# Optimization experiments

Hardware: AMD Instinct MI355X
Metric: run time of the kernel (lower is better)

The kernel has to match this reference:

```python
import jax, jax.numpy as jnp
import numpy as np

V, E = 50000, 300        # vocab, word2vec embedding dim
B, T = 64, 512           # batch, sequence length
U1, U2, DD = 64, 32, 32  # brnn1 units, brnn2 units, dense units


def _glorot(k, shape):
    lim = np.sqrt(6.0 / (shape[0] + shape[1])).astype(np.float32)
    return jax.random.uniform(k, shape, jnp.float32, -lim, lim)


def setup_inputs() -> dict:
    key = jax.random.key(0)
    ks = jax.random.split(key, 12)
    return {
        "token_ids": jax.random.randint(ks[0], (B, T), 0, V),
        "emb": jax.random.normal(ks[1], (V, E), jnp.float32) * 0.05,
        # per-cell gate weights stacked [f|i|c|o] along output dim (same math as 4 separate matmuls)
        "w1f": _glorot(ks[2], (E + U1, 4 * U1)), "b1f": jnp.zeros((4 * U1,), jnp.float32),
        "w1b": _glorot(ks[3], (E + U1, 4 * U1)), "b1b": jnp.zeros((4 * U1,), jnp.float32),
        "w2f": _glorot(ks[4], (2 * U1 + U2, 4 * U2)), "b2f": jnp.zeros((4 * U2,), jnp.float32),
        "w2b": _glorot(ks[5], (2 * U1 + U2, 4 * U2)), "b2b": jnp.zeros((4 * U2,), jnp.float32),
        "wd": _glorot(ks[6], (2 * U2, DD)), "bd": jnp.zeros((DD,), jnp.float32),
        "wo": _glorot(ks[7], (DD, 1)), "bo": jnp.zeros((1,), jnp.float32),
    }


def _lstm(xs, W, b, units, reverse=False):
    # xs: (T, B, D). Single fused gate matmul per step; scan carries (h, c).
    h0 = jnp.zeros((xs.shape[1], units), xs.dtype)
    c0 = jnp.zeros_like(h0)

    def step(carry, x_t):
        h, c = carry
        z = jnp.concatenate([x_t, h], axis=-1) @ W + b  # (B, 4U)
        f, i, g, o = jnp.split(z, 4, axis=-1)
        f = jax.nn.sigmoid(f)
        i = jax.nn.sigmoid(i)
        g = jnp.tanh(g)
        o = jax.nn.sigmoid(o)
        c_new = f * c + i * g
        h_new = o * jnp.tanh(c_new)
        return (h_new, c_new), h_new

    (hT, _), ys = jax.lax.scan(step, (h0, c0), xs, reverse=reverse)
    return ys, hT  # ys: (T, B, U) in original time order; hT = final hidden


def reference(token_ids, emb, w1f, b1f, w1b, b1b, w2f, b2f, w2b, b2b, wd, bd, wo, bo):
    x = emb[token_ids]                      # (B, T, E) frozen word2vec lookup
    xs = jnp.transpose(x, (1, 0, 2))        # (T, B, E)
    # BRNN layer 1: return_sequences=True, merge='concat'
    yf, _ = _lstm(xs, w1f, b1f, U1)
    yb, _ = _lstm(xs, w1b, b1b, U1, reverse=True)
    h1 = jnp.concatenate([yf, yb], axis=-1)  # (T, B, 2*U1); dropout1 = identity at inference
    # BRNN layer 2: return_sequences=False -> final fwd h and final bwd h, concat
    _, hf = _lstm(h1, w2f, b2f, U2)
    _, hb = _lstm(h1, w2b, b2b, U2, reverse=True)
    h2 = jnp.concatenate([hf, hb], axis=-1)  # (B, 2*U2)
    d = jax.nn.relu(h2 @ wd + bd)            # dense head; dropout2 = identity
    return jax.nn.sigmoid(d @ wo + bo)       # (B, 1) sentiment probability
```

## Files before the change

kernel.cpp:

```cpp
#include <hip/hip_runtime.h>

#define T_LEN 512
#define B_SZ  64

typedef _Float16 h2_t  __attribute__((ext_vector_type(2)));
typedef _Float16 f16x8 __attribute__((ext_vector_type(8)));
typedef float    f32x4 __attribute__((ext_vector_type(4)));

#if defined(__has_builtin)
#  if __has_builtin(__builtin_amdgcn_fdot2)
#    define FDOT2(a, b, c) __builtin_amdgcn_fdot2((a), (b), (c), false)
#  endif
#endif
#ifndef FDOT2
__device__ __forceinline__ float fdot2_fb(h2_t a, h2_t b, float c) {
    return fmaf((float)a[0], (float)b[0], fmaf((float)a[1], (float)b[1], c));
}
#  define FDOT2(a, b, c) fdot2_fb((a), (b), (c))
#endif

__device__ __forceinline__ float sigf(float x) {
    return 1.0f / (1.0f + __expf(-x));
}
__device__ __forceinline__ float tanhf_(float x) {
    return 2.0f / (1.0f + __expf(-2.0f * x)) - 1.0f;
}
__device__ __forceinline__ unsigned pack2(float x, float y) {
    h2_t p; p[0] = (_Float16)x; p[1] = (_Float16)y;
    return __builtin_bit_cast(unsigned, p);
}

__device__ __forceinline__ void lds_barrier() {
    asm volatile("s_waitcnt lgkmcnt(0)" ::: "memory");
    __builtin_amdgcn_s_barrier();
    asm volatile("" ::: "memory");
}

__global__ __launch_bounds__(64) void prep_w1(
    const float* __restrict__ w1f, const float* __restrict__ w1b,
    _Float16* __restrict__ Wt1)
{
    const int col = blockIdx.x;
    const int t   = threadIdx.x;
    if (t >= 40) return;
    const float* __restrict__ W = (col < 256) ? w1f : w1b;
    const int c = col & 255;
    f16x8 v;
    #pragma unroll
    for (int i = 0; i < 8; ++i) {
        int k = t * 8 + i;
        float x = (k < 300) ? W[(size_t)k * 256 + c] : 0.0f;
        v[i] = (_Float16)x;
    }
    *(f16x8*)(Wt1 + (size_t)col * 320 + t * 8) = v;
}

__global__ __launch_bounds__(64) void prep_w2(
    const float* __restrict__ w2f, const float* __restrict__ w2b,
    _Float16* __restrict__ Wt2)
{
    const int col = blockIdx.x;
    const int t   = threadIdx.x;
    if (t >= 16) return;
    const float* __restrict__ W = (col < 128) ? w2f : w2b;
    const int c = col & 127;
    f16x8 v;
    #pragma unroll
    for (int i = 0; i < 8; ++i) {
        int k = t * 8 + i;
        v[i] = (_Float16)W[(size_t)k * 128 + c];
    }
    *(f16x8*)(Wt2 + (size_t)col * 128 + t * 8) = v;
}

__global__ __launch_bounds__(256, 1) void gemm1_kernel(
    const int* __restrict__ tok, const float* __restrict__ emb,
    const _Float16* __restrict__ Wt1,
    const float* __restrict__ b1f, const float* __restrict__ b1b,
    float* __restrict__ Z1)
{
    const int row0 = blockIdx.x * 64;
    const int b    = row0 >> 9;
    const int t0   = row0 & 511;
    const int tid  = threadIdx.x;

    __shared__ __align__(16) _Float16 A_lds[64][328];

    {
        const int row = tid >> 2, q = tid & 3;
        const int tk = tok[b * T_LEN + t0 + row];
        const float* __restrict__ src = emb + (size_t)tk * 300 + q * 80;
        #pragma unroll
        for (int i = 0; i < 20; ++i) {
            float4 v;
            if (q == 3 && i >= 15) v = make_float4(0.f, 0.f, 0.f, 0.f);
            else                   v = *(const float4*)(src + i * 4);
            uint2 u; u.x = pack2(v.x, v.y); u.y = pack2(v.z, v.w);
            *(uint2*)&A_lds[row][q * 80 + i * 4] = u;
        }
    }
    __syncthreads();

    const int l   = tid & 63;
    const int w   = tid >> 6;
    const int wN0 = w * 128;
    const int lr  = l & 15;
    const int lk8 = (l >> 4) * 8;

    f32x4 acc[4][8] = {};

    #pragma unroll 2
    for (int ks = 0; ks < 10; ++ks) {
        const int k0 = ks * 32;
        f16x8 af[4];
        #pragma unroll
        for (int m = 0; m < 4; ++m)
            af[m] = *(const f16x8*)&A_lds[m * 16 + lr][k0 + lk8];
        f16x8 bf[8];
        #pragma unroll
        for (int n = 0; n < 8; ++n)
            bf[n] = *(const f16x8*)(Wt1 + (size_t)(wN0 + n * 16 + lr) * 320 + k0 + lk8);
        #pragma unroll
        for (int m = 0; m < 4; ++m)
            #pragma unroll
            for (int n = 0; n < 8; ++n)
                acc[m][n] = __builtin_amdgcn_mfma_f32_16x16x32_f16(af[m], bf[n], acc[m][n], 0, 0, 0);
    }

    const int dir = wN0 >> 8;
    const int rq  = (l >> 4) * 4;
    #pragma unroll
    for (int n = 0; n < 8; ++n) {
        const int colr = (wN0 + n * 16 + lr) & 255;
        const float bv = dir ? b1b[colr] : b1f[colr];
        #pragma unroll
        for (int m = 0; m < 4; ++m) {
            const size_t rb = (size_t)dir * 32768 + row0 + m * 16 + rq;
            #pragma unroll
            for (int r = 0; r < 4; ++r)
                Z1[(rb + r) * 256 + colr] = acc[m][n][r] + bv;
        }
    }
}

__global__ __launch_bounds__(256, 1) void gemm2_kernel(
    const float* __restrict__ H1,
    const _Float16* __restrict__ Wt2,
    const float* __restrict__ b2f, const float* __restrict__ b2b,
    float* __restrict__ Z2)
{
    const int row0 = blockIdx.x * 64;
    const int tid  = threadIdx.x;

    __shared__ __align__(16) _Float16 A_lds[64][136];

    {
        const int row = tid >> 2, q = tid & 3;
        const float* __restrict__ src = H1 + (size_t)(row0 + row) * 128 + q * 32;
        #pragma unroll
        for (int i = 0; i < 8; ++i) {
            float4 v = *(const float4*)(src + i * 4);
            uint2 u; u.x = pack2(v.x, v.y); u.y = pack2(v.z, v.w);
            *(uint2*)&A_lds[row][q * 32 + i * 4] = u;
        }
    }
    __syncthreads();

    const int l   = tid & 63;
    const int w   = tid >> 6;
    const int wN0 = w * 64;
    const int lr  = l & 15;
    const int lk8 = (l >> 4) * 8;

    f32x4 acc[4][4] = {};

    #pragma unroll
    for (int ks = 0; ks < 4; ++ks) {
        const int k0 = ks * 32;
        f16x8 af[4];
        #pragma unroll
        for (int m = 0; m < 4; ++m)
            af[m] = *(const f16x8*)&A_lds[m * 16 + lr][k0 + lk8];
        f16x8 bf[4];
        #pragma unroll
        for (int n = 0; n < 4; ++n)
            bf[n] = *(const f16x8*)(Wt2 + (size_t)(wN0 + n * 16 + lr) * 128 + k0 + lk8);
        #pragma unroll
        for (int m = 0; m < 4; ++m)
            #pragma unroll
            for (int n = 0; n < 4; ++n)
                acc[m][n] = __builtin_amdgcn_mfma_f32_16x16x32_f16(af[m], bf[n], acc[m][n], 0, 0, 0);
    }

    const int dir = wN0 >> 7;
    const int rq  = (l >> 4) * 4;
    #pragma unroll
    for (int n = 0; n < 4; ++n) {
        const int colr = (wN0 + n * 16 + lr) & 127;
        const float bv = dir ? b2b[colr] : b2f[colr];
        #pragma unroll
        for (int m = 0; m < 4; ++m) {
            const size_t rb = (size_t)dir * 32768 + row0 + m * 16 + rq;
            #pragma unroll
            for (int r = 0; r < 4; ++r)
                Z2[(rb + r) * 128 + colr] = acc[m][n][r] + bv;
        }
    }
}

__global__ __launch_bounds__(256, 1) void lstm1_kernel(
    const float* __restrict__ Z1,
    const float* __restrict__ w1f, const float* __restrict__ w1b,
    float* __restrict__ H1)
{
    const int b   = blockIdx.x & 63;
    const int dir = blockIdx.x >> 6;
    const int tid = threadIdx.x;
    const int w   = tid >> 6;
    const int l   = tid & 63;
    const int ul  = l & 15;
    const int g   = (l >> 4) & 3;
    const int u   = w * 16 + ul;
    const int col = g * 64 + u;
    const float* __restrict__ W = dir ? w1b : w1f;

    h2_t wc[32];
    #pragma unroll
    for (int r = 0; r < 32; ++r) {
        float wa = W[(300 + 2 * r) * 256 + col];
        float wb = W[(301 + 2 * r) * 256 + col];
        h2_t p; p[0] = (_Float16)wa; p[1] = (_Float16)wb;
        wc[r] = p;
    }

    __shared__ __align__(16) _Float16 hbuf[2][64];
    if (g == 0) hbuf[0][u] = (_Float16)0.0f;
    lds_barrier();

    float c = 0.0f;

    const float* __restrict__ zcol =
        Z1 + ((size_t)(dir * 64 + b) * T_LEN) * 256 + col;

    float zr[4];
    #pragma unroll
    for (int q = 0; q < 4; ++q) {
        int t = dir ? (T_LEN - 1 - q) : q;
        zr[q] = zcol[(size_t)t * 256];
    }

    float* __restrict__ hout = H1 + (size_t)b * T_LEN * 128 + dir * 64 + u;

    const bool s0b = (g & 1) != 0, s1b = (g >> 1) != 0;
    const float km  = (g == 2) ? -2.0f : -1.0f;
    const float num = (g == 2) ?  2.0f :  1.0f;
    const float off = (g == 2) ?  1.0f :  0.0f;

    for (int sb = 0; sb < T_LEN; sb += 4) {
        #pragma unroll
        for (int q = 0; q < 4; ++q) {
            const int s = sb + q;
            const uint4* hb = (const uint4*)hbuf[s & 1];
            float a0 = zr[q], a1 = 0.f, a2 = 0.f, a3 = 0.f;
            #pragma unroll
            for (int k = 0; k < 8; ++k) {
                uint4 hq = hb[k];
                h2_t p0 = __builtin_bit_cast(h2_t, hq.x);
                h2_t p1 = __builtin_bit_cast(h2_t, hq.y);
                h2_t p2 = __builtin_bit_cast(h2_t, hq.z);
                h2_t p3 = __builtin_bit_cast(h2_t, hq.w);
                a0 = FDOT2(p0, wc[4 * k + 0], a0);
                a1 = FDOT2(p1, wc[4 * k + 1], a1);
                a2 = FDOT2(p2, wc[4 * k + 2], a2);
                a3 = FDOT2(p3, wc[4 * k + 3], a3);
            }
            float zz = (a0 + a1) + (a2 + a3);

            {
                int sp = s + 4; if (sp > T_LEN - 1) sp = T_LEN - 1;
                int tp = dir ? (T_LEN - 1 - sp) : sp;
                zr[q] = zcol[(size_t)tp * 256];
            }

            float e = __expf(km * zz);
            float A = num / (1.0f + e) - off;
            float B = __shfl_xor(A, 16);
            float C = __shfl_xor(A, 32);
            float D = __shfl_xor(B, 32);
            float f_ = s1b ? (s0b ? D : C) : (s0b ? B : A);
            float i_ = s1b ? (s0b ? C : D) : (s0b ? A : B);
            float g_ = s1b ? (s0b ? B : A) : (s0b ? D : C);
            float o_ = s1b ? (s0b ? A : B) : (s0b ? C : D);
            c = fmaf(f_, c, i_ * g_);
            float h = o_ * tanhf_(c);
            if (g == 0) {
                int t = dir ? (T_LEN - 1 - s) : s;
                hout[(size_t)t * 128] = h;
                hbuf[(s + 1) & 1][u] = (_Float16)h;
            }
            lds_barrier();
        }
    }
}

__global__ __launch_bounds__(128, 1) void lstm2_kernel(
    const float* __restrict__ Z2,
    const float* __restrict__ w2f, const float* __restrict__ w2b,
    float* __restrict__ H2)
{
    const int b   = blockIdx.x & 63;
    const int dir = blockIdx.x >> 6;
    const int tid = threadIdx.x;
    const int w   = tid >> 6;
    const int l   = tid & 63;
    const int ul  = l & 15;
    const int g   = (l >> 4) & 3;
    const int u   = w * 16 + ul;
    const int col = g * 32 + u;
    const float* __restrict__ W = dir ? w2b : w2f;

    h2_t wc[16];
    #pragma unroll
    for (int r = 0; r < 16; ++r) {
        float wa = W[(128 + 2 * r) * 128 + col];
        float wb = W[(129 + 2 * r) * 128 + col];
        h2_t p; p[0] = (_Float16)wa; p[1] = (_Float16)wb;
        wc[r] = p;
    }

    __shared__ __align__(16) _Float16 hbuf[2][32];
    if (g == 0) hbuf[0][u] = (_Float16)0.0f;
    lds_barrier();

    float c = 0.0f, h = 0.0f;

    const float* __restrict__ zcol =
        Z2 + ((size_t)(dir * 64 + b) * T_LEN) * 128 + col;

    float zr[4];
    #pragma unroll
    for (int q = 0; q < 4; ++q) {
        int t = dir ? (T_LEN - 1 - q) : q;
        zr[q] = zcol[(size_t)t * 128];
    }

    const bool s0b = (g & 1) != 0, s1b = (g >> 1) != 0;
    const float km  = (g == 2) ? -2.0f : -1.0f;
    const float num = (g == 2) ?  2.0f :  1.0f;
    const float off = (g == 2) ?  1.0f :  0.0f;

    for (int sb = 0; sb < T_LEN; sb += 4) {
        #pragma unroll
        for (int q = 0; q < 4; ++q) {
            const int s = sb + q;
            const uint4* hb = (const uint4*)hbuf[s & 1];
            float a0 = zr[q], a1 = 0.f, a2 = 0.f, a3 = 0.f;
            #pragma unroll
            for (int k = 0; k < 4; ++k) {
                uint4 hq = hb[k];
                h2_t p0 = __builtin_bit_cast(h2_t, hq.x);
                h2_t p1 = __builtin_bit_cast(h2_t, hq.y);
                h2_t p2 = __builtin_bit_cast(h2_t, hq.z);
                h2_t p3 = __builtin_bit_cast(h2_t, hq.w);
                a0 = FDOT2(p0, wc[4 * k + 0], a0);
                a1 = FDOT2(p1, wc[4 * k + 1], a1);
                a2 = FDOT2(p2, wc[4 * k + 2], a2);
                a3 = FDOT2(p3, wc[4 * k + 3], a3);
            }
            float zz = (a0 + a1) + (a2 + a3);

            {
                int sp = s + 4; if (sp > T_LEN - 1) sp = T_LEN - 1;
                int tp = dir ? (T_LEN - 1 - sp) : sp;
                zr[q] = zcol[(size_t)tp * 128];
            }

            float e = __expf(km * zz);
            float A = num / (1.0f + e) - off;
            float B = __shfl_xor(A, 16);
            float C = __shfl_xor(A, 32);
            float D = __shfl_xor(B, 32);
            float f_ = s1b ? (s0b ? D : C) : (s0b ? B : A);
            float i_ = s1b ? (s0b ? C : D) : (s0b ? A : B);
            float g_ = s1b ? (s0b ? B : A) : (s0b ? D : C);
            float o_ = s1b ? (s0b ? A : B) : (s0b ? C : D);
            c = fmaf(f_, c, i_ * g_);
            h = o_ * tanhf_(c);
            if (g == 0)
                hbuf[(s + 1) & 1][u] = (_Float16)h;
            lds_barrier();
        }
    }
    if (g == 0)
        H2[b * 64 + dir * 32 + u] = h;
}

__global__ __launch_bounds__(256) void head_kernel(
    const float* __restrict__ H2,
    const float* __restrict__ wd, const float* __restrict__ bd,
    const float* __restrict__ wo, const float* __restrict__ bo,
    float* __restrict__ out)
{
    const int tid = threadIdx.x;
    const int b = tid >> 2, qd = tid & 3;

    float hv[64];
    #pragma unroll
    for (int v = 0; v < 64; ++v) hv[v] = H2[b * 64 + v];

    float part = 0.0f;
    #pragma unroll
    for (int iq = 0; iq < 8; ++iq) {
        int i = qd * 8 + iq;
        float a = bd[i];
        #pragma unroll
        for (int v = 0; v < 64; ++v)
            a = fmaf(hv[v], wd[v * 32 + i], a);
        a = fmaxf(a, 0.0f);
        part = fmaf(a, wo[i], part);
    }

    __shared__ float ps[256];
    ps[tid] = part;
    __syncthreads();
    if (qd == 0) {
        float s = ps[tid] + ps[tid + 1] + ps[tid + 2] + ps[tid + 3];
        out[b] = sigf(s + bo[0]);
    }
}

extern "C" void kernel_launch(void* const* d_in, const int* in_sizes, int n_in,
                              void* d_out, int out_size, void* d_ws, size_t ws_size,
                              hipStream_t stream)
{
    const int*   tok = (const int*)  d_in[0];
    const float* emb = (const float*)d_in[1];
    const float* w1f = (const float*)d_in[2];
    const float* b1f = (const float*)d_in[3];
    const float* w1b = (const float*)d_in[4];
    const float* b1b = (const float*)d_in[5];
    const float* w2f = (const float*)d_in[6];
    const float* b2f = (const float*)d_in[7];
    const float* w2b = (const float*)d_in[8];
    const float* b2b = (const float*)d_in[9];
    const float* wd  = (const float*)d_in[10];
    const float* bd  = (const float*)d_in[11];
    const float* wo  = (const float*)d_in[12];
    const float* bo  = (const float*)d_in[13];
    float* out = (float*)d_out;

    float* Z1 = (float*)d_ws;
    float* H1 = Z1 + (size_t)2 * 64 * 512 * 256;
    float* H2 = H1 + (size_t)64 * 512 * 128;
    _Float16* Wt1 = (_Float16*)(H2 + 4096);
    _Float16* Wt2 = Wt1 + (size_t)512 * 320;
    float* Z2 = Z1;

    prep_w1<<<512, 64, 0, stream>>>(w1f, w1b, Wt1);
    prep_w2<<<256, 64, 0, stream>>>(w2f, w2b, Wt2);
    gemm1_kernel<<<512, 256, 0, stream>>>(tok, emb, Wt1, b1f, b1b, Z1);
    lstm1_kernel<<<128, 256, 0, stream>>>(Z1, w1f, w1b, H1);
    gemm2_kernel<<<512, 256, 0, stream>>>(H1, Wt2, b2f, b2b, Z2);
    lstm2_kernel<<<128, 128, 0, stream>>>(Z2, w2f, w2b, H2);
    head_kernel<<<1, 256, 0, stream>>>(H2, wd, bd, wo, bo, out);
}
```

Baseline: 424.7 us.

## Batch LSTM recurrences over 16 sequences with MFMA and gate-interleaved Z layout

```diff
diff --git a/kernel.cpp b/kernel.cpp
--- a/kernel.cpp
+++ b/kernel.cpp
@@ -1,24 +1,11 @@
 #include <hip/hip_runtime.h>
 
 #define T_LEN 512
-#define B_SZ  64
 
 typedef _Float16 h2_t  __attribute__((ext_vector_type(2)));
 typedef _Float16 f16x8 __attribute__((ext_vector_type(8)));
 typedef float    f32x4 __attribute__((ext_vector_type(4)));
 
-#if defined(__has_builtin)
-#  if __has_builtin(__builtin_amdgcn_fdot2)
-#    define FDOT2(a, b, c) __builtin_amdgcn_fdot2((a), (b), (c), false)
-#  endif
-#endif
-#ifndef FDOT2
-__device__ __forceinline__ float fdot2_fb(h2_t a, h2_t b, float c) {
-    return fmaf((float)a[0], (float)b[0], fmaf((float)a[1], (float)b[1], c));
-}
-#  define FDOT2(a, b, c) fdot2_fb((a), (b), (c))
-#endif
-
 __device__ __forceinline__ float sigf(float x) {
     return 1.0f / (1.0f + __expf(-x));
 }
@@ -28,6 +15,9 @@
 __device__ __forceinline__ unsigned pack2(float x, float y) {
     h2_t p; p[0] = (_Float16)x; p[1] = (_Float16)y;
     return __builtin_bit_cast(unsigned, p);
+}
+__device__ __forceinline__ f32x4 c4(float4 v) {
+    f32x4 r; r[0] = v.x; r[1] = v.y; r[2] = v.z; r[3] = v.w; return r;
 }
 
 __device__ __forceinline__ void lds_barrier() {
@@ -73,11 +63,36 @@
     *(f16x8*)(Wt2 + (size_t)col * 128 + t * 8) = v;
 }
 
+__global__ __launch_bounds__(64) void prep_whr1(
+    const float* __restrict__ w1f, const float* __restrict__ w1b,
+    _Float16* __restrict__ Whr1)
+{
+    const int x    = blockIdx.x;
+    const int dir  = x >> 8, colp = x & 255;
+    const int u = colp >> 2, g = colp & 3;
+    const int k = threadIdx.x;
+    const float* __restrict__ W = dir ? w1b : w1f;
+    Whr1[(size_t)x * 64 + k] = (_Float16)W[(size_t)(300 + k) * 256 + g * 64 + u];
+}
+
+__global__ __launch_bounds__(64) void prep_whr2(
+    const float* __restrict__ w2f, const float* __restrict__ w2b,
+    _Float16* __restrict__ Whr2)
+{
+    const int x    = blockIdx.x;
+    const int dir  = x >> 7, colp = x & 127;
+    const int u = colp >> 2, g = colp & 3;
+    const int k = threadIdx.x;
+    if (k >= 32) return;
+    const float* __restrict__ W = dir ? w2b : w2f;
+    Whr2[(size_t)x * 32 + k] = (_Float16)W[(size_t)(128 + k) * 128 + g * 32 + u];
+}
+
 __global__ __launch_bounds__(256, 1) void gemm1_kernel(
     const int* __restrict__ tok, const float* __restrict__ emb,
     const _Float16* __restrict__ Wt1,
     const float* __restrict__ b1f, const float* __restrict__ b1b,
-    float* __restrict__ Z1)
+    float* __restrict__ Z1p)
 {
     const int row0 = blockIdx.x * 64;
     const int b    = row0 >> 9;
@@ -128,41 +143,43 @@
     }
 
     const int dir = wN0 >> 8;
+    const int bg  = b >> 4, b16 = b & 15;
     const int rq  = (l >> 4) * 4;
+    float* __restrict__ zslab =
+        Z1p + (((size_t)(dir * 4 + bg) * 512 + t0) * 16 + b16) * 256;
     #pragma unroll
     for (int n = 0; n < 8; ++n) {
         const int colr = (wN0 + n * 16 + lr) & 255;
+        const int uu = colr & 63, gg = colr >> 6;
+        const int colp = uu * 4 + gg;
         const float bv = dir ? b1b[colr] : b1f[colr];
         #pragma unroll
-        for (int m = 0; m < 4; ++m) {
-            const size_t rb = (size_t)dir * 32768 + row0 + m * 16 + rq;
+        for (int m = 0; m < 4; ++m)
             #pragma unroll
             for (int r = 0; r < 4; ++r)
-                Z1[(rb + r) * 256 + colr] = acc[m][n][r] + bv;
-        }
+                zslab[(size_t)(m * 16 + rq + r) * 4096 + colp] = acc[m][n][r] + bv;
     }
 }
 
 __global__ __launch_bounds__(256, 1) void gemm2_kernel(
-    const float* __restrict__ H1,
+    const _Float16* __restrict__ H1f,
     const _Float16* __restrict__ Wt2,
     const float* __restrict__ b2f, const float* __restrict__ b2b,
-    float* __restrict__ Z2)
+    float* __restrict__ Z2p)
 {
     const int row0 = blockIdx.x * 64;
+    const int b    = row0 >> 9;
+    const int t0   = row0 & 511;
     const int tid  = threadIdx.x;
 
     __shared__ __align__(16) _Float16 A_lds[64][136];
 
     {
         const int row = tid >> 2, q = tid & 3;
-        const float* __restrict__ src = H1 + (size_t)(row0 + row) * 128 + q * 32;
-        #pragma unroll
-        for (int i = 0; i < 8; ++i) {
-            float4 v = *(const float4*)(src + i * 4);
-            uint2 u; u.x = pack2(v.x, v.y); u.y = pack2(v.z, v.w);
-            *(uint2*)&A_lds[row][q * 32 + i * 4] = u;
-        }
+        const _Float16* __restrict__ src = H1f + (size_t)(row0 + row) * 128 + q * 32;
+        #pragma unroll
+        for (int i = 0; i < 4; ++i)
+            *(f16x8*)&A_lds[row][q * 32 + i * 8] = *(const f16x8*)(src + i * 8);
     }
     __syncthreads();
 
@@ -193,206 +210,148 @@
     }
 
     const int dir = wN0 >> 7;
+    const int bg  = b >> 4, b16 = b & 15;
     const int rq  = (l >> 4) * 4;
+    float* __restrict__ zslab =
+        Z2p + (((size_t)(dir * 4 + bg) * 512 + t0) * 16 + b16) * 128;
     #pragma unroll
     for (int n = 0; n < 4; ++n) {
         const int colr = (wN0 + n * 16 + lr) & 127;
+        const int uu = colr & 31, gg = colr >> 5;
+        const int colp = uu * 4 + gg;
         const float bv = dir ? b2b[colr] : b2f[colr];
         #pragma unroll
-        for (int m = 0; m < 4; ++m) {
-            const size_t rb = (size_t)dir * 32768 + row0 + m * 16 + rq;
+        for (int m = 0; m < 4; ++m)
             #pragma unroll
             for (int r = 0; r < 4; ++r)
-                Z2[(rb + r) * 128 + colr] = acc[m][n][r] + bv;
-        }
-    }
-}
-
-__global__ __launch_bounds__(256, 1) void lstm1_kernel(
-    const float* __restrict__ Z1,
-    const float* __restrict__ w1f, const float* __restrict__ w1b,
-    float* __restrict__ H1)
-{
-    const int b   = blockIdx.x & 63;
-    const int dir = blockIdx.x >> 6;
+                zslab[(size_t)(m * 16 + rq + r) * 2048 + colp] = acc[m][n][r] + bv;
+    }
+}
+
+__global__ __launch_bounds__(512, 1) void lstm1_kernel(
+    const float* __restrict__ Z1p,
+    const _Float16* __restrict__ Whr1,
+    _Float16* __restrict__ H1f)
+{
+    const int bg  = blockIdx.x & 3;
+    const int dir = blockIdx.x >> 2;
     const int tid = threadIdx.x;
     const int w   = tid >> 6;
     const int l   = tid & 63;
-    const int ul  = l & 15;
-    const int g   = (l >> 4) & 3;
-    const int u   = w * 16 + ul;
-    const int col = g * 64 + u;
-    const float* __restrict__ W = dir ? w1b : w1f;
-
-    h2_t wc[32];
-    #pragma unroll
-    for (int r = 0; r < 32; ++r) {
-        float wa = W[(300 + 2 * r) * 256 + col];
-        float wb = W[(301 + 2 * r) * 256 + col];
-        h2_t p; p[0] = (_Float16)wa; p[1] = (_Float16)wb;
-        wc[r] = p;
-    }
-
-    __shared__ __align__(16) _Float16 hbuf[2][64];
-    if (g == 0) hbuf[0][u] = (_Float16)0.0f;
+    const int bb  = l & 15;
+    const int q   = l >> 4;
+
+    f16x8 af[2][2];
+    #pragma unroll
+    for (int tt = 0; tt < 2; ++tt) {
+        const int colp = (2 * w + tt) * 16 + bb;
+        #pragma unroll
+        for (int ks = 0; ks < 2; ++ks)
+            af[tt][ks] = *(const f16x8*)&Whr1[(size_t)(dir * 256 + colp) * 64 + ks * 32 + q * 8];
+    }
+
+    __shared__ __align__(16) _Float16 hbuf[2][16][72];
+    for (int i = tid; i < 2 * 16 * 72; i += 512) ((_Float16*)hbuf)[i] = (_Float16)0.0f;
     lds_barrier();
 
-    float c = 0.0f;
-
-    const float* __restrict__ zcol =
-        Z1 + ((size_t)(dir * 64 + b) * T_LEN) * 256 + col;
-
-    float zr[4];
-    #pragma unroll
-    for (int q = 0; q < 4; ++q) {
-        int t = dir ? (T_LEN - 1 - q) : q;
-        zr[q] = zcol[(size_t)t * 256];
-    }
-
-    float* __restrict__ hout = H1 + (size_t)b * T_LEN * 128 + dir * 64 + u;
-
-    const bool s0b = (g & 1) != 0, s1b = (g >> 1) != 0;
-    const float km  = (g == 2) ? -2.0f : -1.0f;
-    const float num = (g == 2) ?  2.0f :  1.0f;
-    const float off = (g == 2) ?  1.0f :  0.0f;
-
-    for (int sb = 0; sb < T_LEN; sb += 4) {
-        #pragma unroll
-        for (int q = 0; q < 4; ++q) {
-            const int s = sb + q;
-            const uint4* hb = (const uint4*)hbuf[s & 1];
-            float a0 = zr[q], a1 = 0.f, a2 = 0.f, a3 = 0.f;
-            #pragma unroll
-            for (int k = 0; k < 8; ++k) {
-                uint4 hq = hb[k];
-                h2_t p0 = __builtin_bit_cast(h2_t, hq.x);
-                h2_t p1 = __builtin_bit_cast(h2_t, hq.y);
-                h2_t p2 = __builtin_bit_cast(h2_t, hq.z);
-                h2_t p3 = __builtin_bit_cast(h2_t, hq.w);
-                a0 = FDOT2(p0, wc[4 * k + 0], a0);
-                a1 = FDOT2(p1, wc[4 * k + 1], a1);
-                a2 = FDOT2(p2, wc[4 * k + 2], a2);
-                a3 = FDOT2(p3, wc[4 * k + 3], a3);
-            }
-            float zz = (a0 + a1) + (a2 + a3);
-
-            {
-                int sp = s + 4; if (sp > T_LEN - 1) sp = T_LEN - 1;
-                int tp = dir ? (T_LEN - 1 - sp) : sp;
-                zr[q] = zcol[(size_t)tp * 256];
-            }
-
-            float e = __expf(km * zz);
-            float A = num / (1.0f + e) - off;
-            float B = __shfl_xor(A, 16);
-            float C = __shfl_xor(A, 32);
-            float D = __shfl_xor(B, 32);
-            float f_ = s1b ? (s0b ? D : C) : (s0b ? B : A);
-            float i_ = s1b ? (s0b ? C : D) : (s0b ? A : B);
-            float g_ = s1b ? (s0b ? B : A) : (s0b ? D : C);
-            float o_ = s1b ? (s0b ? A : B) : (s0b ? C : D);
-            c = fmaf(f_, c, i_ * g_);
-            float h = o_ * tanhf_(c);
-            if (g == 0) {
-                int t = dir ? (T_LEN - 1 - s) : s;
-                hout[(size_t)t * 128] = h;
-                hbuf[(s + 1) & 1][u] = (_Float16)h;
-            }
-            lds_barrier();
+    float cc0 = 0.0f, cc1 = 0.0f;
+
+    const size_t dslab = (size_t)(dir * 4 + bg) * 512;
+    const float* __restrict__ zb0 = Z1p + (dslab * 16 + bb) * 256 + (2 * w) * 16 + q * 4;
+    const float* __restrict__ zb1 = zb0 + 16;
+
+    float4 zr0[4], zr1[4];
+    #pragma unroll
+    for (int p = 0; p < 4; ++p) {
+        int t = dir ? (T_LEN - 1 - p) : p;
+        zr0[p] = *(const float4*)(zb0 + (size_t)t * 4096);
+        zr1[p] = *(const float4*)(zb1 + (size_t)t * 4096);
+    }
+
+    const int u0 = 8 * w + q, u1 = u0 + 4;
+    _Float16* __restrict__ hO = H1f + ((size_t)(bg * 16 + bb) * T_LEN) * 128 + dir * 64;
+
+    for (int s = 0; s < T_LEN; ++s) {
+        const int par = s & 1;
+        const int t = dir ? (T_LEN - 1 - s) : s;
+        f16x8 B0 = *(const f16x8*)&hbuf[par][bb][q * 8];
+        f16x8 B1 = *(const f16x8*)&hbuf[par][bb][32 + q * 8];
+        const int slot = s & 3;
+        f32x4 acc0 = __builtin_amdgcn_mfma_f32_16x16x32_f16(af[0][0], B0, c4(zr0[slot]), 0, 0, 0);
+        acc0 = __builtin_amdgcn_mfma_f32_16x16x32_f16(af[0][1], B1, acc0, 0, 0, 0);
+        f32x4 acc1 = __builtin_amdgcn_mfma_f32_16x16x32_f16(af[1][0], B0, c4(zr1[slot]), 0, 0, 0);
+        acc1 = __builtin_amdgcn_mfma_f32_16x16x32_f16(af[1][1], B1, acc1, 0, 0, 0);
+        {
+            int sp = s + 4; if (sp > T_LEN - 1) sp = T_LEN - 1;
+            int tp = dir ? (T_LEN - 1 - sp) : sp;
+            zr0[slot] = *(const float4*)(zb0 + (size_t)tp * 4096);
+            zr1[slot] = *(const float4*)(zb1 + (size_t)tp * 4096);
         }
-    }
-}
-
-__global__ __launch_bounds__(128, 1) void lstm2_kernel(
-    const float* __restrict__ Z2,
-    const float* __restrict__ w2f, const float* __restrict__ w2b,
+        float f0 = sigf(acc0[0]), i0 = sigf(acc0[1]), g0 = tanhf_(acc0[2]), o0 = sigf(acc0[3]);
+        cc0 = fmaf(f0, cc0, i0 * g0);
+        float h0 = o0 * tanhf_(cc0);
+        float f1 = sigf(acc1[0]), i1 = sigf(acc1[1]), g1 = tanhf_(acc1[2]), o1 = sigf(acc1[3]);
+        cc1 = fmaf(f1, cc1, i1 * g1);
+        float h1 = o1 * tanhf_(cc1);
+        hO[(size_t)t * 128 + u0] = (_Float16)h0;
+        hO[(size_t)t * 128 + u1] = (_Float16)h1;
+        hbuf[par ^ 1][bb][u0] = (_Float16)h0;
+        hbuf[par ^ 1][bb][u1] = (_Float16)h1;
+        lds_barrier();
+    }
+}
+
+__global__ __launch_bounds__(512, 1) void lstm2_kernel(
+    const float* __restrict__ Z2p,
+    const _Float16* __restrict__ Whr2,
     float* __restrict__ H2)
 {
-    const int b   = blockIdx.x & 63;
-    const int dir = blockIdx.x >> 6;
+    const int bg  = blockIdx.x & 3;
+    const int dir = blockIdx.x >> 2;
     const int tid = threadIdx.x;
     const int w   = tid >> 6;
     const int l   = tid & 63;
-    const int ul  = l & 15;
-    const int g   = (l >> 4) & 3;
-    const int u   = w * 16 + ul;
-    const int col = g * 32 + u;
-    const float* __restrict__ W = dir ? w2b : w2f;
-
-    h2_t wc[16];
-    #pragma unroll
-    for (int r = 0; r < 16; ++r) {
-        float wa = W[(128 + 2 * r) * 128 + col];
-        float wb = W[(129 + 2 * r) * 128 + col];
-        h2_t p; p[0] = (_Float16)wa; p[1] = (_Float16)wb;
-        wc[r] = p;
-    }
-
-    __shared__ __align__(16) _Float16 hbuf[2][32];
-    if (g == 0) hbuf[0][u] = (_Float16)0.0f;
+    const int bb  = l & 15;
+    const int q   = l >> 4;
+
+    const int colp = w * 16 + bb;
+    f16x8 af = *(const f16x8*)&Whr2[(size_t)(dir * 128 + colp) * 32 + q * 8];
+
+    __shared__ __align__(16) _Float16 hbuf[2][16][40];
+    for (int i = tid; i < 2 * 16 * 40; i += 512) ((_Float16*)hbuf)[i] = (_Float16)0.0f;
     lds_barrier();
 
-    float c = 0.0f, h = 0.0f;
-
-    const float* __restrict__ zcol =
-        Z2 + ((size_t)(dir * 64 + b) * T_LEN) * 128 + col;
-
-    float zr[4];
-    #pragma unroll
-    for (int q = 0; q < 4; ++q) {
-        int t = dir ? (T_LEN - 1 - q) : q;
-        zr[q] = zcol[(size_t)t * 128];
-    }
-
-    const bool s0b = (g & 1) != 0, s1b = (g >> 1) != 0;
-    const float km  = (g == 2) ? -2.0f : -1.0f;
-    const float num = (g == 2) ?  2.0f :  1.0f;
-    const float off = (g == 2) ?  1.0f :  0.0f;
-
-    for (int sb = 0; sb < T_LEN; sb += 4) {
-        #pragma unroll
-        for (int q = 0; q < 4; ++q) {
-            const int s = sb + q;
-            const uint4* hb = (const uint4*)hbuf[s & 1];
-            float a0 = zr[q], a1 = 0.f, a2 = 0.f, a3 = 0.f;
-            #pragma unroll
-            for (int k = 0; k < 4; ++k) {
-                uint4 hq = hb[k];
-                h2_t p0 = __builtin_bit_cast(h2_t, hq.x);
-                h2_t p1 = __builtin_bit_cast(h2_t, hq.y);
-                h2_t p2 = __builtin_bit_cast(h2_t, hq.z);
-                h2_t p3 = __builtin_bit_cast(h2_t, hq.w);
-                a0 = FDOT2(p0, wc[4 * k + 0], a0);
-                a1 = FDOT2(p1, wc[4 * k + 1], a1);
-                a2 = FDOT2(p2, wc[4 * k + 2], a2);
-                a3 = FDOT2(p3, wc[4 * k + 3], a3);
-            }
-            float zz = (a0 + a1) + (a2 + a3);
-
-            {
-                int sp = s + 4; if (sp > T_LEN - 1) sp = T_LEN - 1;
-                int tp = dir ? (T_LEN - 1 - sp) : sp;
-                zr[q] = zcol[(size_t)tp * 128];
-            }
-
-            float e = __expf(km * zz);
-            float A = num / (1.0f + e) - off;
-            float B = __shfl_xor(A, 16);
-            float C = __shfl_xor(A, 32);
-            float D = __shfl_xor(B, 32);
-            float f_ = s1b ? (s0b ? D : C) : (s0b ? B : A);
-            float i_ = s1b ? (s0b ? C : D) : (s0b ? A : B);
-            float g_ = s1b ? (s0b ? B : A) : (s0b ? D : C);
-            float o_ = s1b ? (s0b ? A : B) : (s0b ? C : D);
-            c = fmaf(f_, c, i_ * g_);
-            h = o_ * tanhf_(c);
-            if (g == 0)
-                hbuf[(s + 1) & 1][u] = (_Float16)h;
-            lds_barrier();
+    float cc = 0.0f, h = 0.0f;
+
+    const size_t dslab = (size_t)(dir * 4 + bg) * 512;
+    const float* __restrict__ zb = Z2p + (dslab * 16 + bb) * 128 + w * 16 + q * 4;
+
+    float4 zr[4];
+    #pragma unroll
+    for (int p = 0; p < 4; ++p) {
+        int t = dir ? (T_LEN - 1 - p) : p;
+        zr[p] = *(const float4*)(zb + (size_t)t * 2048);
+    }
+
+    const int u = w * 4 + q;
+
+    for (int s = 0; s < T_LEN; ++s) {
+        const int par = s & 1;
+        f16x8 B0 = *(const f16x8*)&hbuf[par][bb][q * 8];
+        const int slot = s & 3;
+        f32x4 acc = __builtin_amdgcn_mfma_f32_16x16x32_f16(af, B0, c4(zr[slot]), 0, 0, 0);
+        {
+            int sp = s + 4; if (sp > T_LEN - 1) sp = T_LEN - 1;
+            int tp = dir ? (T_LEN - 1 - sp) : sp;
+            zr[slot] = *(const float4*)(zb + (size_t)tp * 2048);
         }
-    }
-    if (g == 0)
-        H2[b * 64 + dir * 32 + u] = h;
+        float f = sigf(acc[0]), i = sigf(acc[1]), g = tanhf_(acc[2]), o = sigf(acc[3]);
+        cc = fmaf(f, cc, i * g);
+        h = o * tanhf_(cc);
+        hbuf[par ^ 1][bb][u] = (_Float16)h;
+        lds_barrier();
+    }
+    H2[(size_t)(bg * 16 + bb) * 64 + dir * 32 + u] = h;
 }
 
 __global__ __launch_bounds__(256) void head_kernel(
@@ -449,18 +408,22 @@
     const float* bo  = (const float*)d_in[13];
     float* out = (float*)d_out;
 
-    float* Z1 = (float*)d_ws;
-    float* H1 = Z1 + (size_t)2 * 64 * 512 * 256;
-    float* H2 = H1 + (size_t)64 * 512 * 128;
-    _Float16* Wt1 = (_Float16*)(H2 + 4096);
-    _Float16* Wt2 = Wt1 + (size_t)512 * 320;
-    float* Z2 = Z1;
-
-    prep_w1<<<512, 64, 0, stream>>>(w1f, w1b, Wt1);
-    prep_w2<<<256, 64, 0, stream>>>(w2f, w2b, Wt2);
-    gemm1_kernel<<<512, 256, 0, stream>>>(tok, emb, Wt1, b1f, b1b, Z1);
-    lstm1_kernel<<<128, 256, 0, stream>>>(Z1, w1f, w1b, H1);
-    gemm2_kernel<<<512, 256, 0, stream>>>(H1, Wt2, b2f, b2b, Z2);
-    lstm2_kernel<<<128, 128, 0, stream>>>(Z2, w2f, w2b, H2);
+    float*    Z1p  = (float*)d_ws;
+    _Float16* H1f  = (_Float16*)(Z1p + (size_t)16777216);
+    float*    H2   = (float*)(H1f + (size_t)4194304);
+    _Float16* Wt1  = (_Float16*)(H2 + 4096);
+    _Float16* Wt2  = Wt1 + (size_t)512 * 320;
+    _Float16* Whr1 = Wt2 + (size_t)256 * 128;
+    _Float16* Whr2 = Whr1 + (size_t)512 * 64;
+    float*    Z2p  = Z1p;
+
+    prep_w1  <<<512, 64, 0, stream>>>(w1f, w1b, Wt1);
+    prep_w2  <<<256, 64, 0, stream>>>(w2f, w2b, Wt2);
+    prep_whr1<<<512, 64, 0, stream>>>(w1f, w1b, Whr1);
+    prep_whr2<<<256, 64, 0, stream>>>(w2f, w2b, Whr2);
+    gemm1_kernel<<<512, 256, 0, stream>>>(tok, emb, Wt1, b1f, b1b, Z1p);
+    lstm1_kernel<<<8, 512, 0, stream>>>(Z1p, Whr1, H1f);
+    gemm2_kernel<<<512, 256, 0, stream>>>(H1f, Wt2, b2f, b2b, Z2p);
+    lstm2_kernel<<<8, 512, 0, stream>>>(Z2p, Whr2, H2);
     head_kernel<<<1, 256, 0, stream>>>(H2, wd, bd, wo, bo, out);
 }
```

Result: slower. 1.082 ms (+154.7%).

## Interleave LSTM gate lanes for DPP exchange, store H1 in fp16, prepack recurrent weights

Applied to the files above, without the earlier changes.

```diff
diff --git a/kernel.cpp b/kernel.cpp
--- a/kernel.cpp
+++ b/kernel.cpp
@@ -1,11 +1,32 @@
 #include <hip/hip_runtime.h>
 
 #define T_LEN 512
-#define B_SZ  64
 
 typedef _Float16 h2_t  __attribute__((ext_vector_type(2)));
 typedef _Float16 f16x8 __attribute__((ext_vector_type(8)));
 typedef float    f32x4 __attribute__((ext_vector_type(4)));
+
+__device__ __forceinline__ float sigf(float x) {
+    return 1.0f / (1.0f + __expf(-x));
+}
+__device__ __forceinline__ float tanhf_(float x) {
+    return 2.0f / (1.0f + __expf(-2.0f * x)) - 1.0f;
+}
+__device__ __forceinline__ unsigned pack2(float x, float y) {
+    h2_t p; p[0] = (_Float16)x; p[1] = (_Float16)y;
+    return __builtin_bit_cast(unsigned, p);
+}
+
+__device__ __forceinline__ float dpp_xor1(float x) {
+    int i = __builtin_bit_cast(int, x);
+    i = __builtin_amdgcn_mov_dpp(i, 0xB1, 0xF, 0xF, true);
+    return __builtin_bit_cast(float, i);
+}
+__device__ __forceinline__ float dpp_xor2(float x) {
+    int i = __builtin_bit_cast(int, x);
+    i = __builtin_amdgcn_mov_dpp(i, 0x4E, 0xF, 0xF, true);
+    return __builtin_bit_cast(float, i);
+}
 
 #if defined(__has_builtin)
 #  if __has_builtin(__builtin_amdgcn_fdot2)
@@ -19,17 +40,6 @@
 #  define FDOT2(a, b, c) fdot2_fb((a), (b), (c))
 #endif
 
-__device__ __forceinline__ float sigf(float x) {
-    return 1.0f / (1.0f + __expf(-x));
-}
-__device__ __forceinline__ float tanhf_(float x) {
-    return 2.0f / (1.0f + __expf(-2.0f * x)) - 1.0f;
-}
-__device__ __forceinline__ unsigned pack2(float x, float y) {
-    h2_t p; p[0] = (_Float16)x; p[1] = (_Float16)y;
-    return __builtin_bit_cast(unsigned, p);
-}
-
 __device__ __forceinline__ void lds_barrier() {
     asm volatile("s_waitcnt lgkmcnt(0)" ::: "memory");
     __builtin_amdgcn_s_barrier();
@@ -73,6 +83,31 @@
     *(f16x8*)(Wt2 + (size_t)col * 128 + t * 8) = v;
 }
 
+__global__ __launch_bounds__(64) void prep_whr1(
+    const float* __restrict__ w1f, const float* __restrict__ w1b,
+    _Float16* __restrict__ Whr1)
+{
+    const int x    = blockIdx.x;
+    const int dir  = x >> 8, colp = x & 255;
+    const int u = colp >> 2, g = colp & 3;
+    const int k = threadIdx.x;
+    const float* __restrict__ W = dir ? w1b : w1f;
+    Whr1[(size_t)x * 64 + k] = (_Float16)W[(size_t)(300 + k) * 256 + g * 64 + u];
+}
+
+__global__ __launch_bounds__(64) void prep_whr2(
+    const float* __restrict__ w2f, const float* __restrict__ w2b,
+    _Float16* __restrict__ Whr2)
+{
+    const int x    = blockIdx.x;
+    const int dir  = x >> 7, colp = x & 127;
+    const int u = colp >> 2, g = colp & 3;
+    const int k = threadIdx.x;
+    if (k >= 32) return;
+    const float* __restrict__ W = dir ? w2b : w2f;
+    Whr2[(size_t)x * 32 + k] = (_Float16)W[(size_t)(128 + k) * 128 + g * 32 + u];
+}
+
 __global__ __launch_bounds__(256, 1) void gemm1_kernel(
     const int* __restrict__ tok, const float* __restrict__ emb,
     const _Float16* __restrict__ Wt1,
@@ -144,7 +179,7 @@
 }
 
 __global__ __launch_bounds__(256, 1) void gemm2_kernel(
-    const float* __restrict__ H1,
+    const _Float16* __restrict__ H1f,
     const _Float16* __restrict__ Wt2,
     const float* __restrict__ b2f, const float* __restrict__ b2b,
     float* __restrict__ Z2)
@@ -156,13 +191,10 @@
 
     {
         const int row = tid >> 2, q = tid & 3;
-        const float* __restrict__ src = H1 + (size_t)(row0 + row) * 128 + q * 32;
-        #pragma unroll
-        for (int i = 0; i < 8; ++i) {
-            float4 v = *(const float4*)(src + i * 4);
-            uint2 u; u.x = pack2(v.x, v.y); u.y = pack2(v.z, v.w);
-            *(uint2*)&A_lds[row][q * 32 + i * 4] = u;
-        }
+        const _Float16* __restrict__ src = H1f + (size_t)(row0 + row) * 128 + q * 32;
+        #pragma unroll
+        for (int i = 0; i < 4; ++i)
+            *(f16x8*)&A_lds[row][q * 32 + i * 8] = *(const f16x8*)(src + i * 8);
     }
     __syncthreads();
 
@@ -210,31 +242,34 @@
 
 __global__ __launch_bounds__(256, 1) void lstm1_kernel(
     const float* __restrict__ Z1,
-    const float* __restrict__ w1f, const float* __restrict__ w1b,
-    float* __restrict__ H1)
+    const _Float16* __restrict__ Whr1,
+    _Float16* __restrict__ H1f)
 {
     const int b   = blockIdx.x & 63;
     const int dir = blockIdx.x >> 6;
     const int tid = threadIdx.x;
     const int w   = tid >> 6;
     const int l   = tid & 63;
-    const int ul  = l & 15;
-    const int g   = (l >> 4) & 3;
-    const int u   = w * 16 + ul;
+    const int g   = l & 3;
+    const int u   = w * 16 + (l >> 2);
     const int col = g * 64 + u;
-    const float* __restrict__ W = dir ? w1b : w1f;
 
     h2_t wc[32];
-    #pragma unroll
-    for (int r = 0; r < 32; ++r) {
-        float wa = W[(300 + 2 * r) * 256 + col];
-        float wb = W[(301 + 2 * r) * 256 + col];
-        h2_t p; p[0] = (_Float16)wa; p[1] = (_Float16)wb;
-        wc[r] = p;
+    {
+        const _Float16* __restrict__ wp = Whr1 + (size_t)(dir * 256 + w * 64 + l) * 64;
+        #pragma unroll
+        for (int r8 = 0; r8 < 8; ++r8) {
+            f16x8 v = *(const f16x8*)(wp + r8 * 8);
+            #pragma unroll
+            for (int j = 0; j < 4; ++j) {
+                h2_t p; p[0] = v[2 * j]; p[1] = v[2 * j + 1];
+                wc[r8 * 4 + j] = p;
+            }
+        }
     }
 
     __shared__ __align__(16) _Float16 hbuf[2][64];
-    if (g == 0) hbuf[0][u] = (_Float16)0.0f;
+    if (tid < 64) { hbuf[0][tid] = (_Float16)0.0f; hbuf[1][tid] = (_Float16)0.0f; }
     lds_barrier();
 
     float c = 0.0f;
@@ -249,7 +284,7 @@
         zr[q] = zcol[(size_t)t * 256];
     }
 
-    float* __restrict__ hout = H1 + (size_t)b * T_LEN * 128 + dir * 64 + u;
+    _Float16* __restrict__ hout = H1f + (size_t)b * T_LEN * 128 + dir * 64 + u;
 
     const bool s0b = (g & 1) != 0, s1b = (g >> 1) != 0;
     const float km  = (g == 2) ? -2.0f : -1.0f;
@@ -284,19 +319,20 @@
 
             float e = __expf(km * zz);
             float A = num / (1.0f + e) - off;
-            float B = __shfl_xor(A, 16);
-            float C = __shfl_xor(A, 32);
-            float D = __shfl_xor(B, 32);
+            float B = dpp_xor1(A);
+            float C = dpp_xor2(A);
+            float D = dpp_xor2(B);
             float f_ = s1b ? (s0b ? D : C) : (s0b ? B : A);
             float i_ = s1b ? (s0b ? C : D) : (s0b ? A : B);
             float g_ = s1b ? (s0b ? B : A) : (s0b ? D : C);
             float o_ = s1b ? (s0b ? A : B) : (s0b ? C : D);
             c = fmaf(f_, c, i_ * g_);
             float h = o_ * tanhf_(c);
+            _Float16 h16 = (_Float16)h;
             if (g == 0) {
                 int t = dir ? (T_LEN - 1 - s) : s;
-                hout[(size_t)t * 128] = h;
-                hbuf[(s + 1) & 1][u] = (_Float16)h;
+                hout[(size_t)t * 128] = h16;
+                hbuf[(s + 1) & 1][u] = h16;
             }
             lds_barrier();
         }
@@ -305,7 +341,7 @@
 
 __global__ __launch_bounds__(128, 1) void lstm2_kernel(
     const float* __restrict__ Z2,
-    const float* __restrict__ w2f, const float* __restrict__ w2b,
+    const _Float16* __restrict__ Whr2,
     float* __restrict__ H2)
 {
     const int b   = blockIdx.x & 63;
@@ -313,23 +349,26 @@
     const int tid = threadIdx.x;
     const int w   = tid >> 6;
     const int l   = tid & 63;
-    const int ul  = l & 15;
-    const int g   = (l >> 4) & 3;
-    const int u   = w * 16 + ul;
+    const int g   = l & 3;
+    const int u   = w * 16 + (l >> 2);
     const int col = g * 32 + u;
-    const float* __restrict__ W = dir ? w2b : w2f;
 
     h2_t wc[16];
-    #pragma unroll
-    for (int r = 0; r < 16; ++r) {
-        float wa = W[(128 + 2 * r) * 128 + col];
-        float wb = W[(129 + 2 * r) * 128 + col];
-        h2_t p; p[0] = (_Float16)wa; p[1] = (_Float16)wb;
-        wc[r] = p;
+    {
+        const _Float16* __restrict__ wp = Whr2 + (size_t)(dir * 128 + w * 64 + l) * 32;
+        #pragma unroll
+        for (int r8 = 0; r8 < 4; ++r8) {
+            f16x8 v = *(const f16x8*)(wp + r8 * 8);
+            #pragma unroll
+            for (int j = 0; j < 4; ++j) {
+                h2_t p; p[0] = v[2 * j]; p[1] = v[2 * j + 1];
+                wc[r8 * 4 + j] = p;
+            }
+        }
     }
 
     __shared__ __align__(16) _Float16 hbuf[2][32];
-    if (g == 0) hbuf[0][u] = (_Float16)0.0f;
+    if (tid < 32) { hbuf[0][tid] = (_Float16)0.0f; hbuf[1][tid] = (_Float16)0.0f; }
     lds_barrier();
 
     float c = 0.0f, h = 0.0f;
@@ -377,9 +416,9 @@
 
             float e = __expf(km * zz);
             float A = num / (1.0f + e) - off;
-            float B = __shfl_xor(A, 16);
-            float C = __shfl_xor(A, 32);
-            float D = __shfl_xor(B, 32);
+            float B = dpp_xor1(A);
+            float C = dpp_xor2(A);
+            float D = dpp_xor2(B);
             float f_ = s1b ? (s0b ? D : C) : (s0b ? B : A);
             float i_ = s1b ? (s0b ? C : D) : (s0b ? A : B);
             float g_ = s1b ? (s0b ? B : A) : (s0b ? D : C);
@@ -449,18 +488,22 @@
     const float* bo  = (const float*)d_in[13];
     float* out = (float*)d_out;
 
-    float* Z1 = (float*)d_ws;
-    float* H1 = Z1 + (size_t)2 * 64 * 512 * 256;
-    float* H2 = H1 + (size_t)64 * 512 * 128;
-    _Float16* Wt1 = (_Float16*)(H2 + 4096);
-    _Float16* Wt2 = Wt1 + (size_t)512 * 320;
-    float* Z2 = Z1;
-
-    prep_w1<<<512, 64, 0, stream>>>(w1f, w1b, Wt1);
-    prep_w2<<<256, 64, 0, stream>>>(w2f, w2b, Wt2);
+    float*    Z1   = (float*)d_ws;
+    _Float16* H1f  = (_Float16*)(Z1 + (size_t)16777216);
+    float*    H2   = (float*)(H1f + (size_t)4194304);
+    _Float16* Wt1  = (_Float16*)(H2 + 4096);
+    _Float16* Wt2  = Wt1 + (size_t)512 * 320;
+    _Float16* Whr1 = Wt2 + (size_t)256 * 128;
+    _Float16* Whr2 = Whr1 + (size_t)512 * 64;
+    float*    Z2   = Z1;
+
+    prep_w1  <<<512, 64, 0, stream>>>(w1f, w1b, Wt1);
+    prep_w2  <<<256, 64, 0, stream>>>(w2f, w2b, Wt2);
+    prep_whr1<<<512, 64, 0, stream>>>(w1f, w1b, Whr1);
+    prep_whr2<<<256, 64, 0, stream>>>(w2f, w2b, Whr2);
     gemm1_kernel<<<512, 256, 0, stream>>>(tok, emb, Wt1, b1f, b1b, Z1);
-    lstm1_kernel<<<128, 256, 0, stream>>>(Z1, w1f, w1b, H1);
-    gemm2_kernel<<<512, 256, 0, stream>>>(H1, Wt2, b2f, b2b, Z2);
-    lstm2_kernel<<<128, 128, 0, stream>>>(Z2, w2f, w2b, H2);
+    lstm1_kernel<<<128, 256, 0, stream>>>(Z1, Whr1, H1f);
+    gemm2_kernel<<<512, 256, 0, stream>>>(H1f, Wt2, b2f, b2b, Z2);
+    lstm2_kernel<<<128, 128, 0, stream>>>(Z2, Whr2, H2);
     head_kernel<<<1, 256, 0, stream>>>(H2, wd, bd, wo, bo, out);
 }
```

After: 367.9 us. -13.4%, faster.
